# Kernel optimization log

Measured on AMD Instinct MI355X. Metric: run time of the kernel, lower is better.

The kernel has to match this reference:

```python
import jax, jax.numpy as jnp
import numpy as np

INNER_LR_INIT = 0.01


def _batched_mlp_logit(fw, x, gate):
    # fw: tuple of per-example weights; x: [B, x_dim]; gate: [B, H]
    fc1, b1, fc2, b2, fc3, b3, fc4 = fw
    h = jax.nn.relu(jnp.einsum('bnm,bm->bn', fc1, x) + b1)
    h = jax.nn.relu(jnp.einsum('bnm,bm->bn', fc2, h) + b2)
    h = jax.nn.relu(jnp.einsum('bnm,bm->bn', fc3, h) + b3)
    h = h * gate
    return jnp.einsum('bnm,bm->bn', fc4, h)  # [B, y_dim]


def setup_inputs() -> dict:
    key = jax.random.key(0)
    B, T, L, X, H, Y = 16, 16, 128, 256, 512, 256
    ks = jax.random.split(key, 10)

    def xavier(k, shape):
        std = (2.0 / (shape[0] + shape[1])) ** 0.5
        return jax.random.normal(k, shape, jnp.float32) * std

    return {
        'train_x': jax.random.normal(ks[0], (B, T, X), jnp.float32),
        'train_y': jax.random.normal(ks[1], (B, T, Y), jnp.float32),
        'test_x': jax.random.normal(ks[2], (B, L, X), jnp.float32),
        'test_y': jax.random.normal(ks[3], (B, L, Y), jnp.float32),
        'train_gate': jax.random.uniform(ks[4], (B, T, H), jnp.float32),
        'test_gate': jax.random.uniform(ks[5], (B, L, H), jnp.float32),
        'fc1': xavier(ks[6], (H, X)), 'b1': jnp.zeros((H,), jnp.float32),
        'fc2': xavier(ks[7], (H, H)), 'b2': jnp.zeros((H,), jnp.float32),
        'fc3': xavier(ks[8], (H, H)), 'b3': jnp.zeros((H,), jnp.float32),
        'fc4': xavier(ks[9], (Y, H)),
        'inner_log_lr': jnp.asarray(np.log(INNER_LR_INIT), jnp.float32),
        'evaluate': 0,
    }


def reference(train_x, train_y, test_x, test_y, train_gate, test_gate,
              fc1, b1, fc2, b2, fc3, b3, fc4, inner_log_lr, evaluate):
    B = train_x.shape[0]
    inner_lr = jnp.exp(inner_log_lr)

    # Replicate shared params into per-example fast weights (MAML).
    fw0 = tuple(jnp.broadcast_to(p, (B,) + p.shape)
                for p in (fc1, b1, fc2, b2, fc3, b3, fc4))

    def inner_loss(fw, x, y, gate):
        logit = _batched_mlp_logit(fw, x, gate)
        return jnp.mean((logit - y) ** 2, axis=-1).sum()

    def step(fw, batch):
        x, y, g = batch
        grads = jax.grad(inner_loss)(fw, x, y, g)
        fw = tuple(w - inner_lr * gr for w, gr in zip(fw, grads))
        return fw, None

    xs = (jnp.swapaxes(train_x, 0, 1),   # [T, B, X]
          jnp.swapaxes(train_y, 0, 1),   # [T, B, Y]
          jnp.swapaxes(train_gate, 0, 1))  # [T, B, H]
    fw, _ = jax.lax.scan(step, fw0, xs)

    fc1b, b1b, fc2b, b2b, fc3b, b3b, fc4b = fw
    h = jax.nn.relu(jnp.einsum('bnm,blm->bln', fc1b, test_x) + b1b[:, None, :])
    h = jax.nn.relu(jnp.einsum('bnm,blm->bln', fc2b, h) + b2b[:, None, :])
    h = jax.nn.relu(jnp.einsum('bnm,blm->bln', fc3b, h) + b3b[:, None, :])
    h = h * test_gate
    logit = jnp.einsum('bnm,blm->bln', fc4b, h)  # [B, L, Y]

    logit_flat = logit.reshape(-1, logit.shape[-1])  # [(B L), Y]
    ty = test_y.reshape(-1, test_y.shape[-1])
    loss = jnp.mean((logit_flat - ty) ** 2, axis=-1)  # [(B L)]
    evaluation = jax.lax.stop_gradient(loss)
    loss = loss.reshape(B, -1, 1)  # [B, L, 1]
    return loss, inner_lr, evaluation, logit_flat
```

## Files before the change

kernel.cpp:

```cpp
#include <hip/hip_runtime.h>
#include <math.h>

#define TB 16
#define TT 16
#define LL 128
#define XX 256
#define HH 512
#define YY 256

#define PW 588
#define SENTU 0xFFC0DEADu

typedef unsigned long long u64;

__device__ __forceinline__ void axs(float* p, float v) {
    (void)__hip_atomic_exchange(p, v, __ATOMIC_RELAXED, __HIP_MEMORY_SCOPE_AGENT);
}
__device__ __forceinline__ float ald(const float* p) {
    return __hip_atomic_load(p, __ATOMIC_RELAXED, __HIP_MEMORY_SCOPE_AGENT);
}
__device__ __forceinline__ unsigned aldu(const unsigned* p) {
    return __hip_atomic_load(p, __ATOMIC_RELAXED, __HIP_MEMORY_SCOPE_AGENT);
}
__device__ __forceinline__ u64 ald8(const u64* p) {
    return __hip_atomic_load(p, __ATOMIC_RELAXED, __HIP_MEMORY_SCOPE_AGENT);
}

__device__ __forceinline__ void partials32L(const float* hist, int tmax,
                                            float* cpw, int blk, const float* sout) {
    const int tid = threadIdx.x;
    const int s2 = tid >> 4, i = tid & 15;
    float pp = 0.f;
    const bool act = (s2 <= tmax);
    if (act) {
        pp = hist[s2 * 32 + 2 * i] * sout[2 * i] +
             hist[s2 * 32 + 2 * i + 1] * sout[2 * i + 1];
    }
    pp += __shfl_xor(pp, 1);
    pp += __shfl_xor(pp, 2);
    pp += __shfl_xor(pp, 4);
    pp += __shfl_xor(pp, 8);
    if (act && i == 0) axs(&cpw[s2 * 16 + blk], pp);
}

__device__ __forceinline__ void partials16L(const float* hist, int tmax,
                                            float* cpw, int blk, const float* sout) {
    const int tid = threadIdx.x;
    const int s2 = tid >> 4, i = tid & 15;
    float pp = 0.f;
    const bool act = (s2 <= tmax);
    if (act) pp = hist[s2 * 16 + i] * sout[i];
    pp += __shfl_xor(pp, 1);
    pp += __shfl_xor(pp, 2);
    pp += __shfl_xor(pp, 4);
    pp += __shfl_xor(pp, 8);
    if (act && i == 0) axs(&cpw[s2 * 16 + blk], pp);
}

template <int MODE>
__device__ __forceinline__ void do_stage(
    int t, float lr, int base, int base16, int blk,
    const float* __restrict__ M, const float* __restrict__ src,
    float* __restrict__ dst, float* __restrict__ dst2,
    const float* __restrict__ tyb, const float* __restrict__ tgb, float rbias,
    float* __restrict__ cw, const float* __restrict__ crd,
    float* s_v, float* sp, float* sout, float* s_c,
    float* hcorr, float* hpart, float* hself,
    float* hD1v, float* hZ1v, float* sG1v)
{
    const int tid = threadIdx.x;
    constexpr int ROWS = (MODE == 2) ? 16 : 32;
    constexpr int G = 256 / ROWS;
    constexpr int KTOT = (MODE == 3) ? 256 : 512;
    constexpr int KPG = KTOT / G;
    constexpr int LD = (MODE == 2) ? YY : HH;

    const int r = tid & (ROWS - 1);
    const int j = tid / ROWS;

    const float* col = M + (j * KPG) * LD + r;
    float wreg[KPG];
    #pragma unroll
    for (int k = 0; k < KPG; ++k) wreg[k] = col[k * LD];

    constexpr float P1 = (MODE == 0 || MODE == 1) ? 1.0f : 0.0f;
    constexpr int NF = (MODE == 3) ? YY : HH;
    {
        const int cs = tid >> 3, cj = tid & 7;
        const bool haveC = (tid < 128) && (cs < t);
        const unsigned* cp = (const unsigned*)(crd + cs * 16 + 2 * cj);
        const unsigned* vp = (const unsigned*)src;
        unsigned c0 = 0u, c1 = 0u, v1 = 0u;
        unsigned v0 = aldu(vp + tid);
        if (NF == 512) v1 = aldu(vp + tid + 256);
        if (haveC) { c0 = aldu(cp); c1 = aldu(cp + 1); }
        while ((v0 == SENTU) | ((NF == 512) & (v1 == SENTU)) |
               (haveC & ((c0 == SENTU) | (c1 == SENTU)))) {
            __builtin_amdgcn_s_sleep(1);
            if (v0 == SENTU) v0 = aldu(vp + tid);
            if (NF == 512 && v1 == SENTU) v1 = aldu(vp + tid + 256);
            if (haveC && c0 == SENTU) c0 = aldu(cp);
            if (haveC && c1 == SENTU) c1 = aldu(cp + 1);
        }
        s_v[tid] = __uint_as_float(v0);
        if (NF == 512) s_v[tid + 256] = __uint_as_float(v1);
        if (tid < 128) {
            float v = haveC ? (__uint_as_float(c0) + __uint_as_float(c1)) : 0.f;
            v += __shfl_xor(v, 1);
            v += __shfl_xor(v, 2);
            v += __shfl_xor(v, 4);
            if (cj == 0) s_c[cs] = lr * (v + P1);
        }
    }
    __syncthreads();

    float a = 0.f;
    const float* vv = s_v + j * KPG;
    #pragma unroll
    for (int k = 0; k < KPG; ++k) a += wreg[k] * vv[k];
    const int lane = tid & 63, w = tid >> 6;
    float sres = 0.f;
    if constexpr (ROWS == 32) {
        a += __shfl_xor(a, 32);
        if (lane < 32) sp[w * 32 + lane] = a;
        __syncthreads();
        if (tid < 32) sres = sp[tid] + sp[32 + tid] + sp[64 + tid] + sp[96 + tid];
    } else {
        a += __shfl_xor(a, 16);
        a += __shfl_xor(a, 32);
        if (lane < 16) sp[w * 16 + lane] = a;
        __syncthreads();
        if (tid < 16) sres = sp[tid] + sp[16 + tid] + sp[32 + tid] + sp[48 + tid];
    }

    if (tid < ROWS) {
        float corr = 0.f;
        for (int s = 0; s < t; ++s) corr += hcorr[s * ROWS + tid] * s_c[s];
        if constexpr (MODE == 5) {
            const float dz = (sres - corr) * ((hcorr[t * 32 + tid] > 0.f) ? 1.f : 0.f);
            axs(dst + t * HH + base + tid, dz);
            hD1v[t * 32 + tid] = dz;
            if (t + 1 < TT) {
                float cr = dz * sG1v[t * 16 + (t + 1)];
                for (int s = 0; s < t; ++s)
                    cr += hD1v[s * 32 + tid] * sG1v[s * 16 + (t + 1)];
                const float h1n = fmaxf(hZ1v[(t + 1) * 32 + tid] - lr * cr, 0.f);
                axs(dst2 + (t + 1) * HH + base + tid, h1n);
                hself[(t + 1) * 32 + tid] = h1n;
                sout[tid] = h1n;
            }
        } else {
            float v;
            if constexpr (MODE == 0)
                v = fmaxf(sres + rbias - corr, 0.f);
            else if constexpr (MODE == 1)
                v = fmaxf(sres + rbias - corr, 0.f) * tgb[t * HH + base + tid];
            else if constexpr (MODE == 2)
                v = (sres - corr - tyb[t * YY + base16 + tid]) * (2.0f / YY);
            else if constexpr (MODE == 3)
                v = (sres - corr) * tgb[t * HH + base + tid] *
                    ((hcorr[t * 32 + tid] > 0.f) ? 1.f : 0.f);
            else
                v = (sres - corr) * ((hcorr[t * 32 + tid] > 0.f) ? 1.f : 0.f);
            if constexpr (MODE == 2) axs(dst + t * YY + base16 + tid, v);
            else                     axs(dst + t * HH + base + tid, v);
            hself[t * ROWS + tid] = v;
            sout[tid] = v;
        }
    }
    __syncthreads();

    const int tmax = (MODE == 5) ? ((t + 1 < TT) ? t : -1) : (t - 1);
    if constexpr (MODE == 2) partials16L(hpart, tmax, cw, blk, sout);
    else                     partials32L(hpart, tmax, cw, blk, sout);
    __syncthreads();
}

__global__ __launch_bounds__(256) void k_tr(
    const float* __restrict__ W1, const float* __restrict__ W2,
    const float* __restrict__ W3, const float* __restrict__ W4,
    float* __restrict__ WT1, float* __restrict__ WT2,
    float* __restrict__ WT3, float* __restrict__ WT4,
    const float* __restrict__ loglr, float* __restrict__ out,
    unsigned* __restrict__ hist0, unsigned* __restrict__ cpart0)
{
    const int tid = threadIdx.x;
    int bid = blockIdx.x;
    if (blockIdx.x == 0 && tid == 0) out[2048] = expf(loglr[0]);

    {
        const int gt = blockIdx.x * 256 + tid;
        for (long i = gt; i < 851968; i += 192 * 256) hist0[i] = SENTU;
        for (long i = gt; i < 393216; i += 192 * 256) cpart0[i] = SENTU;
    }

    const float* src; float* dst; int R, C;
    if (bid < 32)       { src = W1; dst = WT1; R = 512; C = 256; }
    else if (bid < 96)  { src = W2; dst = WT2; R = 512; C = 512; bid -= 32; }
    else if (bid < 160) { src = W3; dst = WT3; R = 512; C = 512; bid -= 96; }
    else                { src = W4; dst = WT4; R = 256; C = 512; bid -= 160; }
    const int tilesC = C >> 6;
    const int i0 = (bid / tilesC) * 64, j0 = (bid % tilesC) * 64;

    __shared__ float sm[64][65];
    #pragma unroll
    for (int rep = 0; rep < 16; ++rep) {
        const int flat = rep * 256 + tid;
        const int r = flat >> 6, c = flat & 63;
        sm[r][c] = src[(i0 + r) * C + j0 + c];
    }
    __syncthreads();
    #pragma unroll
    for (int rep = 0; rep < 16; ++rep) {
        const int flat = rep * 256 + tid;
        const int c = flat >> 6, r = flat & 63;
        dst[(j0 + c) * R + i0 + r] = sm[r][c];
    }
}

__global__ __launch_bounds__(256, 1) void k_inner(
    const float* __restrict__ tx, const float* __restrict__ ty, const float* __restrict__ tg,
    const float* __restrict__ b1v, const float* __restrict__ b2v, const float* __restrict__ b3v,
    const float* __restrict__ W2, const float* __restrict__ W3, const float* __restrict__ W4,
    const float* __restrict__ WT1, const float* __restrict__ WT2, const float* __restrict__ WT3,
    const float* __restrict__ WT4, const float* __restrict__ loglr,
    float* __restrict__ H1, float* __restrict__ H2, float* __restrict__ HG,
    float* __restrict__ D1, float* __restrict__ D2, float* __restrict__ D3, float* __restrict__ D4,
    float* __restrict__ cpart)
{
    const int tid = threadIdx.x;
    const int lane = tid & 63, w = tid >> 6;
    const int g = blockIdx.x;
    const int b = g >> 4;
    const int blk = ((g & 7) << 1) | ((g >> 3) & 1);
    const int base = blk * 32, base16 = blk * 16;
    const float lr = expf(loglr[0]);

    const float* txb = tx + b * (TT * XX);
    const float* tyb = ty + b * (TT * YY);
    const float* tgb = tg + b * (TT * HH);
    float* H1b = H1 + b * (TT * HH);
    float* H2b = H2 + b * (TT * HH);
    float* HGb = HG + b * (TT * HH);
    float* D1b = D1 + b * (TT * HH);
    float* D2b = D2 + b * (TT * HH);
    float* D3b = D3 + b * (TT * HH);
    float* D4b = D4 + b * (TT * YY);
    float* creg = cpart + (long)b * 96 * 256;

    __shared__ float s_x[16 * 260];
    __shared__ float spz[2176];
    __shared__ __align__(16) float s_v[HH];
    __shared__ float sp[128];
    __shared__ float sout[32];
    __shared__ float s_c[16];
    __shared__ float hH1[TT * 32], hH2[TT * 32], hHG[TT * 32];
    __shared__ float hD1[TT * 32], hD2[TT * 32], hD3[TT * 32];
    __shared__ float hD4[TT * 16];
    __shared__ float hZ1[TT * 32];
    __shared__ float sG1[TT * 16];

    const float rb2 = (tid < 32) ? b2v[base + tid] : 0.f;
    const float rb3 = (tid < 32) ? b3v[base + tid] : 0.f;

    {
        const float4* src4 = (const float4*)txb;
        #pragma unroll
        for (int q = 0; q < 4; ++q) {
            const int idx = q * 256 + tid;
            const int tt = idx >> 6, k4 = idx & 63;
            *(float4*)&s_x[tt * 260 + k4 * 4] = src4[idx];
        }
    }
    __syncthreads();
    {
        const int r = tid & 31, j = tid >> 5;
        float acc[16];
        #pragma unroll
        for (int tt = 0; tt < 16; ++tt) acc[tt] = 0.f;
        const float* col = WT1 + (j * 32) * HH + base + r;
        #pragma unroll 4
        for (int kk = 0; kk < 32; ++kk) {
            const float wv = col[kk * HH];
            const int k = j * 32 + kk;
            #pragma unroll
            for (int tt = 0; tt < 16; ++tt) acc[tt] += wv * s_x[tt * 260 + k];
        }
        #pragma unroll
        for (int tt = 0; tt < 16; ++tt) {
            float a = acc[tt] + __shfl_xor(acc[tt], 32);
            if (lane < 32) spz[w * 544 + lane * 17 + tt] = a;
        }
        __syncthreads();
        const int rr = tid & 31, tp = tid >> 5;
        #pragma unroll
        for (int q = 0; q < 2; ++q) {
            const int tt = tp * 2 + q;
            const int row = base + rr;
            float v = spz[rr * 17 + tt] + spz[544 + rr * 17 + tt] +
                      spz[1088 + rr * 17 + tt] + spz[1632 + rr * 17 + tt];
            v += b1v[row];
            hZ1[tt * 32 + rr] = v;
            if (tt == 0) {
                const float h = fmaxf(v, 0.f);
                hH1[rr] = h;
                axs(&H1b[row], h);
            }
        }
    }
    {
        const int ss = tid >> 4, uu = tid & 15;
        float a = 0.f;
        for (int k = 0; k < 256; ++k) a += s_x[ss * 260 + k] * s_x[uu * 260 + k];
        sG1[ss * 16 + uu] = a + 1.0f;
    }
    __syncthreads();

    int k = 0;
    #pragma unroll 1
    for (int t = 0; t < TT; ++t) {
        do_stage<0>(t, lr, base, base16, blk, WT2 + base, H1b + t * HH,
                    H2b, nullptr, tyb, tgb, rb2,
                    creg + (long)k * 256, creg + (long)(k ? k - 1 : 0) * 256,
                    s_v, sp, sout, s_c, hD2, hH2, hH2, hD1, hZ1, sG1);
        ++k;
        do_stage<1>(t, lr, base, base16, blk, WT3 + base, H2b + t * HH,
                    HGb, nullptr, tyb, tgb, rb3,
                    creg + (long)k * 256, creg + (long)(k - 1) * 256,
                    s_v, sp, sout, s_c, hD3, hHG, hHG, hD1, hZ1, sG1);
        ++k;
        do_stage<2>(t, lr, base, base16, blk, WT4 + base16, HGb + t * HH,
                    D4b, nullptr, tyb, tgb, 0.f,
                    creg + (long)k * 256, creg + (long)(k - 1) * 256,
                    s_v, sp, sout, s_c, hD4, hD4, hD4, hD1, hZ1, sG1);
        ++k;
        do_stage<3>(t, lr, base, base16, blk, W4 + base, D4b + t * YY,
                    D3b, nullptr, tyb, tgb, 0.f,
                    creg + (long)k * 256, creg + (long)(k - 1) * 256,
                    s_v, sp, sout, s_c, hHG, hD3, hD3, hD1, hZ1, sG1);
        ++k;
        do_stage<4>(t, lr, base, base16, blk, W3 + base, D3b + t * HH,
                    D2b, nullptr, tyb, tgb, 0.f,
                    creg + (long)k * 256, creg + (long)(k - 1) * 256,
                    s_v, sp, sout, s_c, hH2, hD2, hD2, hD1, hZ1, sG1);
        ++k;
        do_stage<5>(t, lr, base, base16, blk, W2 + base, D2b + t * HH,
                    D1b, H1b, tyb, tgb, 0.f,
                    creg + (long)k * 256, creg + (long)(k - 1) * 256,
                    s_v, sp, sout, s_c, hH1, hH1, hH1, hD1, hZ1, sG1);
        ++k;
    }
}

template <int K, int OUT, bool RELU, bool BIAS, bool PLUSONE>
__device__ __forceinline__ void p2_layer(
    const float* __restrict__ WT,
    const float* __restrict__ bias,
    const float* __restrict__ Dj,
    const float* __restrict__ Asrc,
    float lr, float* sact, float* sactN, float* sWA)
{
    constexpr int KE = (K + 16 + 63) & ~63;
    constexpr int KPG = KE / 8;
    constexpr int SAP = K + 4;
    const int tid = threadIdx.x;

    float* sA = sWA;
    {
        constexpr int TOT = 16 * (K / 2);
        constexpr int PER = TOT / 512;
        u64 tmp[PER];
        #pragma unroll
        for (int q = 0; q < PER; ++q)
            tmp[q] = ald8((const u64*)Asrc + tid + q * 512);
        #pragma unroll
        for (int q = 0; q < PER; ++q) {
            const int idx = tid + q * 512;
            const int s = idx / (K / 2), c = idx - s * (K / 2);
            *(u64*)(sA + s * SAP + c * 2) = tmp[q];
        }
    }
    __syncthreads();

    {
        const int s = tid >> 5, lq = tid & 31;
        const int l = lq >> 3, q = lq & 7;
        const float4* av = (const float4*)(sA + s * SAP);
        const float4* xv = (const float4*)(sact + l * PW);
        float a = 0.f;
        for (int k = 0; k < K / 32; ++k) {
            const float4 u = av[k * 8 + q];
            const float4 x = xv[k * 8 + q];
            a += u.x * x.x + u.y * x.y + u.z * x.z + u.w * x.w;
        }
        a += __shfl_xor(a, 1);
        a += __shfl_xor(a, 2);
        a += __shfl_xor(a, 4);
        if (q == 0) sact[l * PW + K + s] = -lr * (a + (PLUSONE ? 1.f : 0.f));
    }
    __syncthreads();

    float* sP = sWA;
    const int r = tid & 63, j = tid >> 6;
    const float* xb = sact + j * KPG;
    for (int nc = 0; nc < OUT / 256; ++nc) {
        const int nq = nc * 256 + r * 4;
        float4 ac0 = {0.f, 0.f, 0.f, 0.f};
        float4 ac1 = {0.f, 0.f, 0.f, 0.f};
        float4 ac2 = {0.f, 0.f, 0.f, 0.f};
        float4 ac3 = {0.f, 0.f, 0.f, 0.f};
        if ((j + 1) * KPG <= K) {
            const float* c0 = WT + (long)(j * KPG) * OUT + nq;
            #pragma unroll 2
            for (int kk = 0; kk < KPG; kk += 4) {
                const float4 wa = *(const float4*)&c0[(long)(kk + 0) * OUT];
                const float4 wb = *(const float4*)&c0[(long)(kk + 1) * OUT];
                const float4 wc = *(const float4*)&c0[(long)(kk + 2) * OUT];
                const float4 wd = *(const float4*)&c0[(long)(kk + 3) * OUT];
                const float4 x0 = *(const float4*)&xb[0 * PW + kk];
                const float4 x1 = *(const float4*)&xb[1 * PW + kk];
                const float4 x2 = *(const float4*)&xb[2 * PW + kk];
                const float4 x3 = *(const float4*)&xb[3 * PW + kk];
                ac0.x += wa.x*x0.x; ac0.x += wb.x*x0.y; ac0.x += wc.x*x0.z; ac0.x += wd.x*x0.w;
                ac0.y += wa.y*x0.x; ac0.y += wb.y*x0.y; ac0.y += wc.y*x0.z; ac0.y += wd.y*x0.w;
                ac0.z += wa.z*x0.x; ac0.z += wb.z*x0.y; ac0.z += wc.z*x0.z; ac0.z += wd.z*x0.w;
                ac0.w += wa.w*x0.x; ac0.w += wb.w*x0.y; ac0.w += wc.w*x0.z; ac0.w += wd.w*x0.w;
                ac1.x += wa.x*x1.x; ac1.x += wb.x*x1.y; ac1.x += wc.x*x1.z; ac1.x += wd.x*x1.w;
                ac1.y += wa.y*x1.x; ac1.y += wb.y*x1.y; ac1.y += wc.y*x1.z; ac1.y += wd.y*x1.w;
                ac1.z += wa.z*x1.x; ac1.z += wb.z*x1.y; ac1.z += wc.z*x1.z; ac1.z += wd.z*x1.w;
                ac1.w += wa.w*x1.x; ac1.w += wb.w*x1.y; ac1.w += wc.w*x1.z; ac1.w += wd.w*x1.w;
                ac2.x += wa.x*x2.x; ac2.x += wb.x*x2.y; ac2.x += wc.x*x2.z; ac2.x += wd.x*x2.w;
                ac2.y += wa.y*x2.x; ac2.y += wb.y*x2.y; ac2.y += wc.y*x2.z; ac2.y += wd.y*x2.w;
                ac2.z += wa.z*x2.x; ac2.z += wb.z*x2.y; ac2.z += wc.z*x2.z; ac2.z += wd.z*x2.w;
                ac2.w += wa.w*x2.x; ac2.w += wb.w*x2.y; ac2.w += wc.w*x2.z; ac2.w += wd.w*x2.w;
                ac3.x += wa.x*x3.x; ac3.x += wb.x*x3.y; ac3.x += wc.x*x3.z; ac3.x += wd.x*x3.w;
                ac3.y += wa.y*x3.x; ac3.y += wb.y*x3.y; ac3.y += wc.y*x3.z; ac3.y += wd.y*x3.w;
                ac3.z += wa.z*x3.x; ac3.z += wb.z*x3.y; ac3.z += wc.z*x3.z; ac3.z += wd.z*x3.w;
                ac3.w += wa.w*x3.x; ac3.w += wb.w*x3.y; ac3.w += wc.w*x3.z; ac3.w += wd.w*x3.w;
            }
        } else {
            #pragma unroll 2
            for (int kk = 0; kk < KPG; kk += 4) {
                float4 wa, wb, wc, wd;
                {
                    const int k0 = j * KPG + kk;
                    wa = (k0 + 0 < K) ? *(const float4*)&WT[(long)(k0 + 0) * OUT + nq]
                       : (k0 + 0 < K + 16) ? make_float4(ald(&Dj[(k0 + 0 - K) * OUT + nq]),
                                                         ald(&Dj[(k0 + 0 - K) * OUT + nq + 1]),
                                                         ald(&Dj[(k0 + 0 - K) * OUT + nq + 2]),
                                                         ald(&Dj[(k0 + 0 - K) * OUT + nq + 3]))
                       : make_float4(0.f, 0.f, 0.f, 0.f);
                    wb = (k0 + 1 < K) ? *(const float4*)&WT[(long)(k0 + 1) * OUT + nq]
                       : (k0 + 1 < K + 16) ? make_float4(ald(&Dj[(k0 + 1 - K) * OUT + nq]),
                                                         ald(&Dj[(k0 + 1 - K) * OUT + nq + 1]),
                                                         ald(&Dj[(k0 + 1 - K) * OUT + nq + 2]),
                                                         ald(&Dj[(k0 + 1 - K) * OUT + nq + 3]))
                       : make_float4(0.f, 0.f, 0.f, 0.f);
                    wc = (k0 + 2 < K) ? *(const float4*)&WT[(long)(k0 + 2) * OUT + nq]
                       : (k0 + 2 < K + 16) ? make_float4(ald(&Dj[(k0 + 2 - K) * OUT + nq]),
                                                         ald(&Dj[(k0 + 2 - K) * OUT + nq + 1]),
                                                         ald(&Dj[(k0 + 2 - K) * OUT + nq + 2]),
                                                         ald(&Dj[(k0 + 2 - K) * OUT + nq + 3]))
                       : make_float4(0.f, 0.f, 0.f, 0.f);
                    wd = (k0 + 3 < K) ? *(const float4*)&WT[(long)(k0 + 3) * OUT + nq]
                       : (k0 + 3 < K + 16) ? make_float4(ald(&Dj[(k0 + 3 - K) * OUT + nq]),
                                                         ald(&Dj[(k0 + 3 - K) * OUT + nq + 1]),
                                                         ald(&Dj[(k0 + 3 - K) * OUT + nq + 2]),
                                                         ald(&Dj[(k0 + 3 - K) * OUT + nq + 3]))
                       : make_float4(0.f, 0.f, 0.f, 0.f);
                }
                const float4 x0 = *(const float4*)&xb[0 * PW + kk];
                const float4 x1 = *(const float4*)&xb[1 * PW + kk];
                const float4 x2 = *(const float4*)&xb[2 * PW + kk];
                const float4 x3 = *(const float4*)&xb[3 * PW + kk];
                ac0.x += wa.x*x0.x; ac0.x += wb.x*x0.y; ac0.x += wc.x*x0.z; ac0.x += wd.x*x0.w;
                ac0.y += wa.y*x0.x; ac0.y += wb.y*x0.y; ac0.y += wc.y*x0.z; ac0.y += wd.y*x0.w;
                ac0.z += wa.z*x0.x; ac0.z += wb.z*x0.y; ac0.z += wc.z*x0.z; ac0.z += wd.z*x0.w;
                ac0.w += wa.w*x0.x; ac0.w += wb.w*x0.y; ac0.w += wc.w*x0.z; ac0.w += wd.w*x0.w;
                ac1.x += wa.x*x1.x; ac1.x += wb.x*x1.y; ac1.x += wc.x*x1.z; ac1.x += wd.x*x1.w;
                ac1.y += wa.y*x1.x; ac1.y += wb.y*x1.y; ac1.y += wc.y*x1.z; ac1.y += wd.y*x1.w;
                ac1.z += wa.z*x1.x; ac1.z += wb.z*x1.y; ac1.z += wc.z*x1.z; ac1.z += wd.z*x1.w;
                ac1.w += wa.w*x1.x; ac1.w += wb.w*x1.y; ac1.w += wc.w*x1.z; ac1.w += wd.w*x1.w;
                ac2.x += wa.x*x2.x; ac2.x += wb.x*x2.y; ac2.x += wc.x*x2.z; ac2.x += wd.x*x2.w;
                ac2.y += wa.y*x2.x; ac2.y += wb.y*x2.y; ac2.y += wc.y*x2.z; ac2.y += wd.y*x2.w;
                ac2.z += wa.z*x2.x; ac2.z += wb.z*x2.y; ac2.z += wc.z*x2.z; ac2.z += wd.z*x2.w;
                ac2.w += wa.w*x2.x; ac2.w += wb.w*x2.y; ac2.w += wc.w*x2.z; ac2.w += wd.w*x2.w;
                ac3.x += wa.x*x3.x; ac3.x += wb.x*x3.y; ac3.x += wc.x*x3.z; ac3.x += wd.x*x3.w;
                ac3.y += wa.y*x3.x; ac3.y += wb.y*x3.y; ac3.y += wc.y*x3.z; ac3.y += wd.y*x3.w;
                ac3.z += wa.z*x3.x; ac3.z += wb.z*x3.y; ac3.z += wc.z*x3.z; ac3.z += wd.z*x3.w;
                ac3.w += wa.w*x3.x; ac3.w += wb.w*x3.y; ac3.w += wc.w*x3.z; ac3.w += wd.w*x3.w;
            }
        }
        __syncthreads();
        {
            float* row = sP + (j * 64 + r) * 17;
            row[0]  = ac0.x; row[1]  = ac0.y; row[2]  = ac0.z; row[3]  = ac0.w;
            row[4]  = ac1.x; row[5]  = ac1.y; row[6]  = ac1.z; row[7]  = ac1.w;
            row[8]  = ac2.x; row[9]  = ac2.y; row[10] = ac2.z; row[11] = ac2.w;
            row[12] = ac3.x; row[13] = ac3.y; row[14] = ac3.z; row[15] = ac3.w;
        }
        __syncthreads();
        {
            #pragma unroll
            for (int e = 0; e < 2; ++e) {
                const int o = tid * 2 + e;
                const int nn = o >> 2, ll = o & 3;
                const int rq = nn >> 2, cq = nn & 3;
                const int off = (ll << 2) + cq;
                float v = 0.f;
                #pragma unroll
                for (int q = 0; q < 8; ++q)
                    v += sP[(q * 64 + rq) * 17 + off];
                const int n = nc * 256 + nn;
                if (BIAS) v += bias[n];
                if (RELU) v = fmaxf(v, 0.f);
                sactN[ll * PW + n] = v;
            }
        }
    }
    __syncthreads();
    constexpr int ZC = PW - (OUT + 16);
    for (int f = tid; f < 4 * ZC; f += 512) {
        const int l = f / ZC, c = f - l * ZC;
        sactN[l * PW + OUT + 16 + c] = 0.f;
    }
    __syncthreads();
}

__global__ __launch_bounds__(512, 4) void k_p2(
    const float* __restrict__ tx, const float* __restrict__ tex,
    const float* __restrict__ tey, const float* __restrict__ teg,
    const float* __restrict__ b1v, const float* __restrict__ b2v,
    const float* __restrict__ b3v,
    const float* __restrict__ WT1, const float* __restrict__ WT2,
    const float* __restrict__ WT3, const float* __restrict__ WT4,
    const float* __restrict__ H1, const float* __restrict__ H2,
    const float* __restrict__ HG,
    const float* __restrict__ D1, const float* __restrict__ D2,
    const float* __restrict__ D3, const float* __restrict__ D4,
    const float* __restrict__ loglr, float* __restrict__ outp)
{
    const int tid = threadIdx.x;
    const int b = blockIdx.x >> 5;
    const int l0 = (blockIdx.x & 31) * 4;
    const float lr = expf(loglr[0]);

    __shared__ __align__(16) float pool[13408];
    float* a0  = pool;
    float* a1  = pool + 2352;
    float* sWA = pool + 4704;

    const float* txb = tx + b * (TT * XX);
    const float* H1b = H1 + b * (TT * HH);
    const float* H2b = H2 + b * (TT * HH);
    const float* HGb = HG + b * (TT * HH);
    const float* D1b = D1 + b * (TT * HH);
    const float* D2b = D2 + b * (TT * HH);
    const float* D3b = D3 + b * (TT * HH);
    const float* D4b = D4 + b * (TT * YY);

    for (int f = tid; f < 4 * PW; f += 512) {
        const int l = f / PW, c = f - l * PW;
        a0[f] = (c < XX) ? tex[((long)b * LL + l0 + l) * XX + c] : 0.f;
    }
    __syncthreads();

    p2_layer<XX, HH, true, true, true>(WT1, b1v, D1b, txb, lr, a0, a1, sWA);
    p2_layer<HH, HH, true, true, true>(WT2, b2v, D2b, H1b, lr, a1, a0, sWA);
    p2_layer<HH, HH, true, true, true>(WT3, b3v, D3b, H2b, lr, a0, a1, sWA);

    for (int f = tid; f < 4 * HH; f += 512) {
        const int l = f >> 9, k = f & 511;
        a1[l * PW + k] *= teg[((long)b * LL + l0 + l) * HH + k];
    }
    __syncthreads();

    p2_layer<HH, YY, false, false, false>(WT4, nullptr, D4b, HGb, lr, a1, a0, sWA);

    for (int f = tid; f < 4 * YY; f += 512) {
        const int l = f >> 8, y = f & 255;
        outp[4097 + ((long)(b * LL + l0 + l)) * YY + y] = a0[l * PW + y];
    }
    if (tid < 128) {
        const int l = tid >> 5, kk = tid & 31;
        float a = 0.f;
        #pragma unroll
        for (int jj = 0; jj < 8; ++jj) {
            const int y = kk * 8 + jj;
            const float d = a0[l * PW + y] -
                            tey[((long)b * LL + l0 + l) * YY + y];
            a += d * d;
        }
        a += __shfl_xor(a, 1);
        a += __shfl_xor(a, 2);
        a += __shfl_xor(a, 4);
        a += __shfl_xor(a, 8);
        a += __shfl_xor(a, 16);
        if (kk == 0) {
            const float v = a * (1.0f / YY);
            const int idx = b * LL + l0 + l;
            outp[idx] = v;
            outp[2049 + idx] = v;
        }
    }
}

extern "C" void kernel_launch(void* const* d_in, const int* in_sizes, int n_in,
                              void* d_out, int out_size, void* d_ws, size_t ws_size,
                              hipStream_t stream)
{
    const float* tx    = (const float*)d_in[0];
    const float* ty    = (const float*)d_in[1];
    const float* tex   = (const float*)d_in[2];
    const float* tey   = (const float*)d_in[3];
    const float* tg    = (const float*)d_in[4];
    const float* teg   = (const float*)d_in[5];
    const float* W1    = (const float*)d_in[6];
    const float* b1    = (const float*)d_in[7];
    const float* W2    = (const float*)d_in[8];
    const float* b2    = (const float*)d_in[9];
    const float* W3    = (const float*)d_in[10];
    const float* b3    = (const float*)d_in[11];
    const float* W4    = (const float*)d_in[12];
    const float* loglr = (const float*)d_in[13];

    float* out = (float*)d_out;
    float* ws  = (float*)d_ws;

    float* H1     = ws + 135168;
    float* H2     = ws + 266240;
    float* HG     = ws + 397312;
    float* D1     = ws + 528384;
    float* D2     = ws + 659456;
    float* D3     = ws + 790528;
    float* D4     = ws + 921600;
    float* ActA   = ws + 1024000;
    float* WT1    = ActA;
    float* WT2    = ActA + 131072;
    float* WT3    = ActA + 393216;
    float* WT4    = ActA + 655360;
    float* cpart  = ws + 2072576;

    k_tr<<<192, 256, 0, stream>>>(W1, W2, W3, W4, WT1, WT2, WT3, WT4, loglr,
                                  out, (unsigned*)H1, (unsigned*)cpart);

    k_inner<<<TB * 16, 256, 0, stream>>>(tx, ty, tg, b1, b2, b3, W2, W3, W4,
                                         WT1, WT2, WT3, WT4, loglr,
                                         H1, H2, HG, D1, D2, D3, D4, cpart);

    k_p2<<<TB * 32, 512, 0, stream>>>(tx, tex, tey, teg, b1, b2, b3,
                                      WT1, WT2, WT3, WT4,
                                      H1, H2, HG, D1, D2, D3, D4,
                                      loglr, out);
}
```

Baseline: 383.0 us.

## Process two batch examples per inner-loop block, halving k_inner grid

Each k_inner block now handles a pair of examples, interleaving their per-stage work in the scan, and the grid shrinks from 256 to 128 blocks. Prologue work is factored into a p0_task helper that runs once per example. The intent is to give each block independent work to overlap while it waits on cross-block partial-sum handoffs, and to cut the number of co-resident spinning blocks. The cost is serialised compute per block and more shared memory, which may lengthen the critical path.

```diff
diff --git a/kernel.cpp b/kernel.cpp
--- a/kernel.cpp
+++ b/kernel.cpp
@@ -176,93 +176,13 @@
     __syncthreads();
 }
 
-__global__ __launch_bounds__(256) void k_tr(
-    const float* __restrict__ W1, const float* __restrict__ W2,
-    const float* __restrict__ W3, const float* __restrict__ W4,
-    float* __restrict__ WT1, float* __restrict__ WT2,
-    float* __restrict__ WT3, float* __restrict__ WT4,
-    const float* __restrict__ loglr, float* __restrict__ out,
-    unsigned* __restrict__ hist0, unsigned* __restrict__ cpart0)
-{
-    const int tid = threadIdx.x;
-    int bid = blockIdx.x;
-    if (blockIdx.x == 0 && tid == 0) out[2048] = expf(loglr[0]);
-
-    {
-        const int gt = blockIdx.x * 256 + tid;
-        for (long i = gt; i < 851968; i += 192 * 256) hist0[i] = SENTU;
-        for (long i = gt; i < 393216; i += 192 * 256) cpart0[i] = SENTU;
-    }
-
-    const float* src; float* dst; int R, C;
-    if (bid < 32)       { src = W1; dst = WT1; R = 512; C = 256; }
-    else if (bid < 96)  { src = W2; dst = WT2; R = 512; C = 512; bid -= 32; }
-    else if (bid < 160) { src = W3; dst = WT3; R = 512; C = 512; bid -= 96; }
-    else                { src = W4; dst = WT4; R = 256; C = 512; bid -= 160; }
-    const int tilesC = C >> 6;
-    const int i0 = (bid / tilesC) * 64, j0 = (bid % tilesC) * 64;
-
-    __shared__ float sm[64][65];
-    #pragma unroll
-    for (int rep = 0; rep < 16; ++rep) {
-        const int flat = rep * 256 + tid;
-        const int r = flat >> 6, c = flat & 63;
-        sm[r][c] = src[(i0 + r) * C + j0 + c];
-    }
-    __syncthreads();
-    #pragma unroll
-    for (int rep = 0; rep < 16; ++rep) {
-        const int flat = rep * 256 + tid;
-        const int c = flat >> 6, r = flat & 63;
-        dst[(j0 + c) * R + i0 + r] = sm[r][c];
-    }
-}
-
-__global__ __launch_bounds__(256, 1) void k_inner(
-    const float* __restrict__ tx, const float* __restrict__ ty, const float* __restrict__ tg,
-    const float* __restrict__ b1v, const float* __restrict__ b2v, const float* __restrict__ b3v,
-    const float* __restrict__ W2, const float* __restrict__ W3, const float* __restrict__ W4,
-    const float* __restrict__ WT1, const float* __restrict__ WT2, const float* __restrict__ WT3,
-    const float* __restrict__ WT4, const float* __restrict__ loglr,
-    float* __restrict__ H1, float* __restrict__ H2, float* __restrict__ HG,
-    float* __restrict__ D1, float* __restrict__ D2, float* __restrict__ D3, float* __restrict__ D4,
-    float* __restrict__ cpart)
+__device__ __forceinline__ void p0_task(
+    const float* __restrict__ txb, const float* __restrict__ WT1,
+    const float* __restrict__ b1v, float* __restrict__ H1b, int base,
+    float* s_x, float* spz, float* hZ1, float* hH1, float* sG1)
 {
     const int tid = threadIdx.x;
     const int lane = tid & 63, w = tid >> 6;
-    const int g = blockIdx.x;
-    const int b = g >> 4;
-    const int blk = ((g & 7) << 1) | ((g >> 3) & 1);
-    const int base = blk * 32, base16 = blk * 16;
-    const float lr = expf(loglr[0]);
-
-    const float* txb = tx + b * (TT * XX);
-    const float* tyb = ty + b * (TT * YY);
-    const float* tgb = tg + b * (TT * HH);
-    float* H1b = H1 + b * (TT * HH);
-    float* H2b = H2 + b * (TT * HH);
-    float* HGb = HG + b * (TT * HH);
-    float* D1b = D1 + b * (TT * HH);
-    float* D2b = D2 + b * (TT * HH);
-    float* D3b = D3 + b * (TT * HH);
-    float* D4b = D4 + b * (TT * YY);
-    float* creg = cpart + (long)b * 96 * 256;
-
-    __shared__ float s_x[16 * 260];
-    __shared__ float spz[2176];
-    __shared__ __align__(16) float s_v[HH];
-    __shared__ float sp[128];
-    __shared__ float sout[32];
-    __shared__ float s_c[16];
-    __shared__ float hH1[TT * 32], hH2[TT * 32], hHG[TT * 32];
-    __shared__ float hD1[TT * 32], hD2[TT * 32], hD3[TT * 32];
-    __shared__ float hD4[TT * 16];
-    __shared__ float hZ1[TT * 32];
-    __shared__ float sG1[TT * 16];
-
-    const float rb2 = (tid < 32) ? b2v[base + tid] : 0.f;
-    const float rb3 = (tid < 32) ? b3v[base + tid] : 0.f;
-
     {
         const float4* src4 = (const float4*)txb;
         #pragma unroll
@@ -315,39 +235,164 @@
         sG1[ss * 16 + uu] = a + 1.0f;
     }
     __syncthreads();
+}
+
+__global__ __launch_bounds__(256) void k_tr(
+    const float* __restrict__ W1, const float* __restrict__ W2,
+    const float* __restrict__ W3, const float* __restrict__ W4,
+    float* __restrict__ WT1, float* __restrict__ WT2,
+    float* __restrict__ WT3, float* __restrict__ WT4,
+    const float* __restrict__ loglr, float* __restrict__ out,
+    unsigned* __restrict__ hist0, unsigned* __restrict__ cpart0)
+{
+    const int tid = threadIdx.x;
+    int bid = blockIdx.x;
+    if (blockIdx.x == 0 && tid == 0) out[2048] = expf(loglr[0]);
+
+    {
+        const int gt = blockIdx.x * 256 + tid;
+        for (long i = gt; i < 851968; i += 192 * 256) hist0[i] = SENTU;
+        for (long i = gt; i < 393216; i += 192 * 256) cpart0[i] = SENTU;
+    }
+
+    const float* src; float* dst; int R, C;
+    if (bid < 32)       { src = W1; dst = WT1; R = 512; C = 256; }
+    else if (bid < 96)  { src = W2; dst = WT2; R = 512; C = 512; bid -= 32; }
+    else if (bid < 160) { src = W3; dst = WT3; R = 512; C = 512; bid -= 96; }
+    else                { src = W4; dst = WT4; R = 256; C = 512; bid -= 160; }
+    const int tilesC = C >> 6;
+    const int i0 = (bid / tilesC) * 64, j0 = (bid % tilesC) * 64;
+
+    __shared__ float sm[64][65];
+    #pragma unroll
+    for (int rep = 0; rep < 16; ++rep) {
+        const int flat = rep * 256 + tid;
+        const int r = flat >> 6, c = flat & 63;
+        sm[r][c] = src[(i0 + r) * C + j0 + c];
+    }
+    __syncthreads();
+    #pragma unroll
+    for (int rep = 0; rep < 16; ++rep) {
+        const int flat = rep * 256 + tid;
+        const int c = flat >> 6, r = flat & 63;
+        dst[(j0 + c) * R + i0 + r] = sm[r][c];
+    }
+}
+
+__global__ __launch_bounds__(256, 1) void k_inner(
+    const float* __restrict__ tx, const float* __restrict__ ty, const float* __restrict__ tg,
+    const float* __restrict__ b1v, const float* __restrict__ b2v, const float* __restrict__ b3v,
+    const float* __restrict__ W2, const float* __restrict__ W3, const float* __restrict__ W4,
+    const float* __restrict__ WT1, const float* __restrict__ WT2, const float* __restrict__ WT3,
+    const float* __restrict__ WT4, const float* __restrict__ loglr,
+    float* __restrict__ H1, float* __restrict__ H2, float* __restrict__ HG,
+    float* __restrict__ D1, float* __restrict__ D2, float* __restrict__ D3, float* __restrict__ D4,
+    float* __restrict__ cpart)
+{
+    const int tid = threadIdx.x;
+    const int g = blockIdx.x;
+    const int blk = ((g & 7) << 1) | ((g >> 3) & 1);
+    const int pr = g >> 4;
+    const int bA = pr * 2, bB = pr * 2 + 1;
+    const int base = blk * 32, base16 = blk * 16;
+    const float lr = expf(loglr[0]);
+
+    const float* tyA = ty + bA * (TT * YY);
+    const float* tgA = tg + bA * (TT * HH);
+    float* H1A = H1 + bA * (TT * HH);
+    float* H2A = H2 + bA * (TT * HH);
+    float* HGA = HG + bA * (TT * HH);
+    float* D1A = D1 + bA * (TT * HH);
+    float* D2A = D2 + bA * (TT * HH);
+    float* D3A = D3 + bA * (TT * HH);
+    float* D4A = D4 + bA * (TT * YY);
+    float* crA = cpart + (long)bA * 96 * 256;
+    const float* tyB = ty + bB * (TT * YY);
+    const float* tgB = tg + bB * (TT * HH);
+    float* H1B = H1 + bB * (TT * HH);
+    float* H2B = H2 + bB * (TT * HH);
+    float* HGB = HG + bB * (TT * HH);
+    float* D1B = D1 + bB * (TT * HH);
+    float* D2B = D2 + bB * (TT * HH);
+    float* D3B = D3 + bB * (TT * HH);
+    float* D4B = D4 + bB * (TT * YY);
+    float* crB = cpart + (long)bB * 96 * 256;
+
+    __shared__ float s_x[16 * 260];
+    __shared__ float spz[2176];
+    __shared__ __align__(16) float s_v[HH];
+    __shared__ float sp[128];
+    __shared__ float sout[32];
+    __shared__ float s_c[16];
+    __shared__ float hH1A[TT * 32], hH2A[TT * 32], hHGA[TT * 32];
+    __shared__ float hD1A[TT * 32], hD2A[TT * 32], hD3A[TT * 32];
+    __shared__ float hD4A[TT * 16], hZ1A[TT * 32], sG1A[TT * 16];
+    __shared__ float hH1B[TT * 32], hH2B[TT * 32], hHGB[TT * 32];
+    __shared__ float hD1B[TT * 32], hD2B[TT * 32], hD3B[TT * 32];
+    __shared__ float hD4B[TT * 16], hZ1B[TT * 32], sG1B[TT * 16];
+
+    const float rb2 = (tid < 32) ? b2v[base + tid] : 0.f;
+    const float rb3 = (tid < 32) ? b3v[base + tid] : 0.f;
+
+    p0_task(tx + bA * (TT * XX), WT1, b1v, H1A, base, s_x, spz, hZ1A, hH1A, sG1A);
+    p0_task(tx + bB * (TT * XX), WT1, b1v, H1B, base, s_x, spz, hZ1B, hH1B, sG1B);
 
     int k = 0;
     #pragma unroll 1
     for (int t = 0; t < TT; ++t) {
-        do_stage<0>(t, lr, base, base16, blk, WT2 + base, H1b + t * HH,
-                    H2b, nullptr, tyb, tgb, rb2,
-                    creg + (long)k * 256, creg + (long)(k ? k - 1 : 0) * 256,
-                    s_v, sp, sout, s_c, hD2, hH2, hH2, hD1, hZ1, sG1);
+        do_stage<0>(t, lr, base, base16, blk, WT2 + base, H1A + t * HH,
+                    H2A, nullptr, tyA, tgA, rb2,
+                    crA + (long)k * 256, crA + (long)(k ? k - 1 : 0) * 256,
+                    s_v, sp, sout, s_c, hD2A, hH2A, hH2A, hD1A, hZ1A, sG1A);
+        do_stage<0>(t, lr, base, base16, blk, WT2 + base, H1B + t * HH,
+                    H2B, nullptr, tyB, tgB, rb2,
+                    crB + (long)k * 256, crB + (long)(k ? k - 1 : 0) * 256,
+                    s_v, sp, sout, s_c, hD2B, hH2B, hH2B, hD1B, hZ1B, sG1B);
         ++k;
-        do_stage<1>(t, lr, base, base16, blk, WT3 + base, H2b + t * HH,
-                    HGb, nullptr, tyb, tgb, rb3,
-                    creg + (long)k * 256, creg + (long)(k - 1) * 256,
-                    s_v, sp, sout, s_c, hD3, hHG, hHG, hD1, hZ1, sG1);
+        do_stage<1>(t, lr, base, base16, blk, WT3 + base, H2A + t * HH,
+                    HGA, nullptr, tyA, tgA, rb3,
+                    crA + (long)k * 256, crA + (long)(k - 1) * 256,
+                    s_v, sp, sout, s_c, hD3A, hHGA, hHGA, hD1A, hZ1A, sG1A);
+        do_stage<1>(t, lr, base, base16, blk, WT3 + base, H2B + t * HH,
+                    HGB, nullptr, tyB, tgB, rb3,
+                    crB + (long)k * 256, crB + (long)(k - 1) * 256,
+                    s_v, sp, sout, s_c, hD3B, hHGB, hHGB, hD1B, hZ1B, sG1B);
         ++k;
-        do_stage<2>(t, lr, base, base16, blk, WT4 + base16, HGb + t * HH,
-                    D4b, nullptr, tyb, tgb, 0.f,
-                    creg + (long)k * 256, creg + (long)(k - 1) * 256,
-                    s_v, sp, sout, s_c, hD4, hD4, hD4, hD1, hZ1, sG1);
+        do_stage<2>(t, lr, base, base16, blk, WT4 + base16, HGA + t * HH,
+                    D4A, nullptr, tyA, tgA, 0.f,
+                    crA + (long)k * 256, crA + (long)(k - 1) * 256,
+                    s_v, sp, sout, s_c, hD4A, hD4A, hD4A, hD1A, hZ1A, sG1A);
+        do_stage<2>(t, lr, base, base16, blk, WT4 + base16, HGB + t * HH,
+                    D4B, nullptr, tyB, tgB, 0.f,
+                    crB + (long)k * 256, crB + (long)(k - 1) * 256,
+                    s_v, sp, sout, s_c, hD4B, hD4B, hD4B, hD1B, hZ1B, sG1B);
         ++k;
-        do_stage<3>(t, lr, base, base16, blk, W4 + base, D4b + t * YY,
-                    D3b, nullptr, tyb, tgb, 0.f,
-                    creg + (long)k * 256, creg + (long)(k - 1) * 256,
-                    s_v, sp, sout, s_c, hHG, hD3, hD3, hD1, hZ1, sG1);
+        do_stage<3>(t, lr, base, base16, blk, W4 + base, D4A + t * YY,
+                    D3A, nullptr, tyA, tgA, 0.f,
+                    crA + (long)k * 256, crA + (long)(k - 1) * 256,
+                    s_v, sp, sout, s_c, hHGA, hD3A, hD3A, hD1A, hZ1A, sG1A);
+        do_stage<3>(t, lr, base, base16, blk, W4 + base, D4B + t * YY,
+                    D3B, nullptr, tyB, tgB, 0.f,
+                    crB + (long)k * 256, crB + (long)(k - 1) * 256,
+                    s_v, sp, sout, s_c, hHGB, hD3B, hD3B, hD1B, hZ1B, sG1B);
         ++k;
-        do_stage<4>(t, lr, base, base16, blk, W3 + base, D3b + t * HH,
-                    D2b, nullptr, tyb, tgb, 0.f,
-                    creg + (long)k * 256, creg + (long)(k - 1) * 256,
-                    s_v, sp, sout, s_c, hH2, hD2, hD2, hD1, hZ1, sG1);
+        do_stage<4>(t, lr, base, base16, blk, W3 + base, D3A + t * HH,
+                    D2A, nullptr, tyA, tgA, 0.f,
+                    crA + (long)k * 256, crA + (long)(k - 1) * 256,
+                    s_v, sp, sout, s_c, hH2A, hD2A, hD2A, hD1A, hZ1A, sG1A);
+        do_stage<4>(t, lr, base, base16, blk, W3 + base, D3B + t * HH,
+                    D2B, nullptr, tyB, tgB, 0.f,
+                    crB + (long)k * 256, crB + (long)(k - 1) * 256,
+                    s_v, sp, sout, s_c, hH2B, hD2B, hD2B, hD1B, hZ1B, sG1B);
         ++k;
-        do_stage<5>(t, lr, base, base16, blk, W2 + base, D2b + t * HH,
-                    D1b, H1b, tyb, tgb, 0.f,
-                    creg + (long)k * 256, creg + (long)(k - 1) * 256,
-                    s_v, sp, sout, s_c, hH1, hH1, hH1, hD1, hZ1, sG1);
+        do_stage<5>(t, lr, base, base16, blk, W2 + base, D2A + t * HH,
+                    D1A, H1A, tyA, tgA, 0.f,
+                    crA + (long)k * 256, crA + (long)(k - 1) * 256,
+                    s_v, sp, sout, s_c, hH1A, hH1A, hH1A, hD1A, hZ1A, sG1A);
+        do_stage<5>(t, lr, base, base16, blk, W2 + base, D2B + t * HH,
+                    D1B, H1B, tyB, tgB, 0.f,
+                    crB + (long)k * 256, crB + (long)(k - 1) * 256,
+                    s_v, sp, sout, s_c, hH1B, hH1B, hH1B, hD1B, hZ1B, sG1B);
         ++k;
     }
 }
@@ -644,9 +689,9 @@
     k_tr<<<192, 256, 0, stream>>>(W1, W2, W3, W4, WT1, WT2, WT3, WT4, loglr,
                                   out, (unsigned*)H1, (unsigned*)cpart);
 
-    k_inner<<<TB * 16, 256, 0, stream>>>(tx, ty, tg, b1, b2, b3, W2, W3, W4,
-                                         WT1, WT2, WT3, WT4, loglr,
-                                         H1, H2, HG, D1, D2, D3, D4, cpart);
+    k_inner<<<128, 256, 0, stream>>>(tx, ty, tg, b1, b2, b3, W2, W3, W4,
+                                     WT1, WT2, WT3, WT4, loglr,
+                                     H1, H2, HG, D1, D2, D3, D4, cpart);
 
     k_p2<<<TB * 32, 512, 0, stream>>>(tx, tex, tey, teg, b1, b2, b3,
                                       WT1, WT2, WT3, WT4,
```

Measured after the change: 488.7 us. +27.6%, slower.
